# Kernel optimization log

Hardware: AMD Instinct MI355X
Metric: run time of the kernel (lower is better)

The kernel has to match this reference:

```python
import jax, jax.numpy as jnp
import numpy as np

B = 2; CIN = 64; COUT = 64; H = 192; W = 192
KH = 3; KW = 3; K = KH * KW; NC = 20
STRIDE = 1; PAD = 1; DIL = 1


def setup_inputs() -> dict:
    key = jax.random.key(0)
    ks = jax.random.split(key, 7)
    x = jax.random.normal(ks[0], (B, CIN, H, W), jnp.float32)
    input_LO = jax.random.uniform(ks[1], (B, NC, H, W), jnp.float32)
    output_LO = jax.random.uniform(ks[2], (B, NC, H, W), jnp.float32)  # HO=H, WO=W for k3 s1 p1
    weight = jax.random.normal(ks[3], (COUT, CIN, KH, KW), jnp.float32) * 0.05
    bias = jax.random.normal(ks[4], (COUT,), jnp.float32) * 0.05
    # conv_offset is zero-init in source; use small random weights so offsets are exercised
    off_w = jax.random.normal(ks[5], (2 * K, CIN, KH, KW), jnp.float32) * 0.01
    off_b = jnp.zeros((2 * K,), jnp.float32)
    return {"x": x, "input_LO": input_LO, "output_LO": output_LO,
            "weight": weight, "bias": bias, "off_w": off_w, "off_b": off_b}


def _gather(img_flat, idx):
    # img_flat: [B, C, H*W], idx: [B, N] -> [B, C, N]
    return jax.vmap(lambda im, ix: im[:, ix])(img_flat, idx)


def _bilinear(img, py, px, zero_pad):
    """Bilinear sample img [B,C,Hi,Wi] at pixel coords py/px [B,K,Ho,Wo].
    zero_pad=True -> zeros outside (deformable conv); False -> border clamp (grid_sample border)."""
    Bb, Cc, Hh, Ww = img.shape
    if not zero_pad:
        px = jnp.clip(px, 0.0, Ww - 1.0)
        py = jnp.clip(py, 0.0, Hh - 1.0)
    x0 = jnp.floor(px)
    y0 = jnp.floor(py)
    img_f = img.reshape(Bb, Cc, Hh * Ww)
    out = jnp.zeros((Bb, Cc) + px.shape[1:], img.dtype)
    for dy in (0.0, 1.0):
        for dx in (0.0, 1.0):
            yc = y0 + dy
            xc = x0 + dx
            w = (1.0 - jnp.abs(py - yc)) * (1.0 - jnp.abs(px - xc))
            if zero_pad:
                valid = (yc >= 0) & (yc <= Hh - 1) & (xc >= 0) & (xc <= Ww - 1)
                w = w * valid.astype(w.dtype)
            yi = jnp.clip(yc, 0, Hh - 1).astype(jnp.int32)
            xi = jnp.clip(xc, 0, Ww - 1).astype(jnp.int32)
            idx = (yi * Ww + xi).reshape(Bb, -1)
            g = _gather(img_f, idx).reshape((Bb, Cc) + px.shape[1:])
            out = out + g * w[:, None]
    return out


def reference(x, input_LO, output_LO, weight, bias, off_w, off_b):
    # 1) offset conv (torch chunk+cat is identity, so offset == conv_offset(x))
    offset = jax.lax.conv_general_dilated(
        x, off_w, (STRIDE, STRIDE), ((PAD, PAD), (PAD, PAD)),
        dimension_numbers=("NCHW", "OIHW", "NCHW")) + off_b[None, :, None, None]
    Bb, _, Ho, Wo = offset.shape
    off = offset.reshape(Bb, K, 2, Ho, Wo)
    off_y = off[:, :, 0]   # channel 2k   -> y offset
    off_x = off[:, :, 1]   # channel 2k+1 -> x offset
    hk = (jnp.arange(K) // KW).astype(x.dtype)[None, :, None, None]
    wk = (jnp.arange(K) % KW).astype(x.dtype)[None, :, None, None]

    # 2) mask: grid_sample label map at deformed locations (align_corners=True, border pad)
    hor = jnp.linspace(-1.0, 1.0, Wo)[None, None, None, :]
    ver = jnp.linspace(-1.0, 1.0, Ho)[None, None, :, None]
    gx = hor * STRIDE - PAD + (wk + off_x) / ((W - 1.0) / 2.0)
    gy = ver * STRIDE - PAD + (hk + off_y) / ((H - 1.0) / 2.0)
    px = (gx + 1.0) * (W - 1.0) / 2.0
    py = (gy + 1.0) * (H - 1.0) / 2.0
    samp_LO = _bilinear(input_LO, py, px, zero_pad=False)        # [B,NC,K,Ho,Wo]
    mask = jnp.einsum("bnkhw,bnhw->bkhw", samp_LO, output_LO)    # [B,K,Ho,Wo]

    # 3) modulated deformable conv (DCNv2 math, zero padding outside)
    base_y = (jnp.arange(Ho) * STRIDE - PAD).astype(x.dtype)[None, None, :, None]
    base_x = (jnp.arange(Wo) * STRIDE - PAD).astype(x.dtype)[None, None, None, :]
    py2 = base_y + hk * DIL + off_y
    px2 = base_x + wk * DIL + off_x
    samp = _bilinear(x, py2, px2, zero_pad=True)                 # [B,C,K,Ho,Wo]
    samp = samp * mask[:, None]
    out = jnp.einsum("bckhw,ock->bohw", samp, weight.reshape(COUT, CIN, K))
    return out + bias[None, :, None, None]
```

## Files before the change

kernel.cpp:

```cpp
#include <hip/hip_runtime.h>

#define Bn   2
#define CIN  64
#define COUT 64
#define Hd   192
#define Wd   192
#define HWd  (Hd*Wd)
#define Kk   9
#define NCh  20
#define NCP  24
#define NTILE 1152

typedef __attribute__((ext_vector_type(8))) short short8;
typedef __attribute__((ext_vector_type(4))) float f32x4;

static __device__ __forceinline__ ushort f2bf(float f) {
    unsigned u = __float_as_uint(f);
    u += 0x7fffu + ((u >> 16) & 1u);
    return (ushort)(u >> 16);
}
static __device__ __forceinline__ float bf2f(ushort v) {
    return __uint_as_float(((unsigned)v) << 16);
}

__global__ __launch_bounds__(256) void kT(const float* __restrict__ x,
        const float* __restrict__ inLO, const float* __restrict__ outLO,
        const float* __restrict__ w, const float* __restrict__ off_w,
        ushort* __restrict__ xtb, ushort* __restrict__ inLOb,
        ushort* __restrict__ outLOb, ushort* __restrict__ wtb,
        ushort* __restrict__ owtb) {
    __shared__ float lds[20 * 257];
    int bid = blockIdx.x, tid = threadIdx.x;
    if (bid < 1152) {
        int b = bid / 576, p0 = (bid % 576) * 64;
        const float* src = x + b * CIN * HWd + p0;
        #pragma unroll
        for (int r = 0; r < 16; ++r) {
            int e = r * 256 + tid;
            int c = e >> 6, p = e & 63;
            lds[c * 65 + p] = src[c * HWd + p];
        }
        __syncthreads();
        ushort* dst = xtb + ((size_t)(b * HWd + p0)) * 64;
        #pragma unroll
        for (int r = 0; r < 16; ++r) {
            int e = r * 256 + tid;
            int p = e >> 6, c = e & 63;
            dst[e] = f2bf(lds[c * 65 + p]);
        }
    } else if (bid < 1728) {
        int q = bid - 1152;
        int t = q / 288; q %= 288;
        int b = q / 144, p0 = (q % 144) * 256;
        const float* src = (t == 0 ? inLO : outLO) + b * NCh * HWd + p0;
        ushort* dst = (t == 0 ? inLOb : outLOb) + ((size_t)(b * HWd + p0)) * NCP;
        #pragma unroll
        for (int r = 0; r < 20; ++r) {
            int e = r * 256 + tid;
            int n = e >> 8, p = e & 255;
            lds[n * 257 + p] = src[n * HWd + p];
        }
        __syncthreads();
        #pragma unroll
        for (int r = 0; r < 24; ++r) {
            int e = r * 256 + tid;
            int p = e / NCP, n = e - p * NCP;
            dst[e] = (n < NCh) ? f2bf(lds[n * 257 + p]) : (ushort)0;
        }
    } else if (bid < 1872) {
        int f = (bid - 1728) * 256 + tid;
        int e = f & 7, lane = (f >> 3) & 63;
        int kt = (f >> 9) & 1, nt = (f >> 10) & 3, tap = f >> 12;
        int o = nt * 16 + (lane & 15);
        int c = kt * 32 + (lane >> 4) * 8 + e;
        wtb[f] = f2bf(w[(o * CIN + c) * Kk + tap]);
    } else {
        int f = (bid - 1872) * 256 + tid;
        if (f < 18432) {
            int e = f & 7, lane = (f >> 3) & 63;
            int kt = (f >> 9) & 1, nt = (f >> 10) & 1, tap = f >> 11;
            int oc = nt * 16 + (lane & 15);
            int c = kt * 32 + (lane >> 4) * 8 + e;
            owtb[f] = (oc < 18) ? f2bf(off_w[(oc * CIN + c) * Kk + tap]) : (ushort)0;
        }
    }
}

__global__ __launch_bounds__(256) void k1_gemm(const ushort* __restrict__ xtb,
        const ushort* __restrict__ owtb, const float* __restrict__ off_b,
        float* __restrict__ off) {
    int tid = threadIdx.x, bid = blockIdx.x;
    int jt = bid % 3, i = (bid / 3) % Hd, b = bid / (3 * Hd);
    int j0 = jt * 64;
    int lane = tid & 63, wv = tid >> 6;
    int m = lane & 15;
    int ch8 = lane >> 4;
    int j = j0 + wv * 16 + m;
    const ushort* xb = xtb + (size_t)b * HWd * 64;

    float bv0 = off_b[m];
    float bv1 = (m < 2) ? off_b[16 + m] : 0.f;
    f32x4 acc0 = (f32x4){bv0, bv0, bv0, bv0};
    f32x4 acc1 = (f32x4){bv1, bv1, bv1, bv1};
    short8 zero8 = {0, 0, 0, 0, 0, 0, 0, 0};

    #pragma unroll
    for (int t = 0; t < 9; ++t) {
        int yy = i + t / 3 - 1;
        int xx = j + t % 3 - 1;
        bool ok = (yy >= 0) && (yy < Hd) && (xx >= 0) && (xx < Wd);
        int yc = min(max(yy, 0), Hd - 1), xc = min(max(xx, 0), Wd - 1);
        const ushort* rowp = xb + (size_t)(yc * Wd + xc) * 64 + ch8 * 8;
        short8 a0 = *(const short8*)rowp;
        short8 a1 = *(const short8*)(rowp + 32);
        a0 = ok ? a0 : zero8;
        a1 = ok ? a1 : zero8;
        const ushort* wb = owtb + ((size_t)t << 11);
        short8 b00 = *(const short8*)(wb + (lane << 3));
        short8 b01 = *(const short8*)(wb + 512 + (lane << 3));
        short8 b10 = *(const short8*)(wb + 1024 + (lane << 3));
        short8 b11 = *(const short8*)(wb + 1536 + (lane << 3));
        acc0 = __builtin_amdgcn_mfma_f32_16x16x32_bf16(a0, b00, acc0, 0, 0, 0);
        acc0 = __builtin_amdgcn_mfma_f32_16x16x32_bf16(a1, b01, acc0, 0, 0, 0);
        acc1 = __builtin_amdgcn_mfma_f32_16x16x32_bf16(a0, b10, acc1, 0, 0, 0);
        acc1 = __builtin_amdgcn_mfma_f32_16x16x32_bf16(a1, b11, acc1, 0, 0, 0);
    }

    int prow = j0 + wv * 16 + (lane >> 4) * 4;
    int oc = lane & 15;
    float* ob = off + (size_t)b * 18 * HWd + i * Wd;
    #pragma unroll
    for (int r = 0; r < 4; ++r)
        ob[oc * HWd + prow + r] = acc0[r];
    if (oc < 2) {
        #pragma unroll
        for (int r = 0; r < 4; ++r)
            ob[(16 + oc) * HWd + prow + r] = acc1[r];
    }
}

__global__ __launch_bounds__(256) void k2_mask(const ushort* __restrict__ inLOb,
        const ushort* __restrict__ outLOb, const float* __restrict__ off,
        float* __restrict__ mask) {
    int t = blockIdx.x * 256 + threadIdx.x;
    int p = t % HWd;
    int k = (t / HWd) % Kk;
    int b = t / (Kk * HWd);
    int j = p % Wd, i = p / Wd;
    float offy = off[(b * 18 + 2 * k) * HWd + p];
    float offx = off[(b * 18 + 2 * k + 1) * HWd + p];
    float py = (float)(i + (k / 3)) + offy - 95.5f;
    float px = (float)(j + (k % 3)) + offx - 95.5f;
    py = fminf(fmaxf(py, 0.f), 191.f);
    px = fminf(fmaxf(px, 0.f), 191.f);
    float y0f = floorf(py), x0f = floorf(px);
    float ly = py - y0f, lx = px - x0f;
    int y0 = (int)y0f, x0 = (int)x0f;
    int y1 = min(y0 + 1, Hd - 1), x1 = min(x0 + 1, Wd - 1);
    float w00 = (1.f - ly) * (1.f - lx);
    float w01 = (1.f - ly) * lx;
    float w10 = ly * (1.f - lx);
    float w11 = ly * lx;
    const short8* L00 = (const short8*)(inLOb + (size_t)(b * HWd + y0 * Wd + x0) * NCP);
    const short8* L01 = (const short8*)(inLOb + (size_t)(b * HWd + y0 * Wd + x1) * NCP);
    const short8* L10 = (const short8*)(inLOb + (size_t)(b * HWd + y1 * Wd + x0) * NCP);
    const short8* L11 = (const short8*)(inLOb + (size_t)(b * HWd + y1 * Wd + x1) * NCP);
    const short8* O  = (const short8*)(outLOb + (size_t)(b * HWd + p) * NCP);
    float acc = 0.f;
    #pragma unroll
    for (int n3 = 0; n3 < 3; ++n3) {
        short8 a = L00[n3], bb = L01[n3], c = L10[n3], d = L11[n3], o = O[n3];
        #pragma unroll
        for (int e = 0; e < 8; ++e) {
            float s = w00 * bf2f((ushort)a[e]) + w01 * bf2f((ushort)bb[e])
                    + w10 * bf2f((ushort)c[e]) + w11 * bf2f((ushort)d[e]);
            acc += s * bf2f((ushort)o[e]);
        }
    }
    mask[(b * Kk + k) * HWd + p] = acc;
}

__global__ __launch_bounds__(256) void k3_part(const ushort* __restrict__ xtb,
        const float* __restrict__ off, const float* __restrict__ mask,
        const ushort* __restrict__ wtb, float* __restrict__ part) {
    __shared__ __align__(16) ushort A_lds[4 * 2 * 64 * 8];
    int tid = threadIdx.x;
    int bid = blockIdx.x;
    int h = bid >= NTILE;
    int tb = bid - (h ? NTILE : 0);
    int t0 = h ? 5 : 0, t1 = h ? 9 : 5;
    int jt = tb % 3, i = (tb / 3) % Hd, b = tb / (3 * Hd);
    int j0 = jt * 64;

    int lane = tid & 63;
    int wv_id = tid >> 6;
    int wm = wv_id >> 1;
    int wn = wv_id & 1;

    int pxo = lane & 7;
    int chunk = lane >> 3;
    int kt_s = chunk >> 2;
    int ksub = chunk & 3;
    const ushort* xb = xtb + (size_t)b * HWd * 64;

    f32x4 acc[2][2];
    #pragma unroll
    for (int mi = 0; mi < 2; ++mi)
        #pragma unroll
        for (int ni = 0; ni < 2; ++ni)
            acc[mi][ni] = (f32x4){0.f, 0.f, 0.f, 0.f};

    for (int t = t0; t < t1; ++t) {
        short8 bf[2][2];
        #pragma unroll
        for (int kt = 0; kt < 2; ++kt)
            #pragma unroll
            for (int ni = 0; ni < 2; ++ni) {
                int nt = wn * 2 + ni;
                bf[kt][ni] = *(const short8*)(wtb +
                    ((((t * 4 + nt) * 2 + kt) * 64 + lane) << 3));
            }

        #pragma unroll
        for (int r = 0; r < 2; ++r) {
            int px_loc = (wv_id << 4) + (r << 3) + pxo;
            int pix = i * Wd + j0 + px_loc;
            float offy = off[(b * 18 + 2 * t) * HWd + pix];
            float offx = off[(b * 18 + 2 * t + 1) * HWd + pix];
            float m = mask[(b * Kk + t) * HWd + pix];
            float py = (float)(i - 1 + (t / 3)) + offy;
            float px = (float)(j0 + px_loc - 1 + (t % 3)) + offx;
            float y0f = floorf(py), x0f = floorf(px);
            float ly = py - y0f, lx = px - x0f;
            int y0 = (int)y0f, x0 = (int)x0f;
            int y1 = y0 + 1, x1 = x0 + 1;
            bool vy0 = (y0 >= 0 && y0 < Hd), vy1 = (y1 >= 0 && y1 < Hd);
            bool vx0 = (x0 >= 0 && x0 < Wd), vx1 = (x1 >= 0 && x1 < Wd);
            float w00 = (vy0 && vx0) ? (1.f - ly) * (1.f - lx) * m : 0.f;
            float w01 = (vy0 && vx1) ? (1.f - ly) * lx * m : 0.f;
            float w10 = (vy1 && vx0) ? ly * (1.f - lx) * m : 0.f;
            float w11 = (vy1 && vx1) ? ly * lx * m : 0.f;
            int y0c = min(max(y0, 0), Hd - 1), y1c = min(max(y1, 0), Hd - 1);
            int x0c = min(max(x0, 0), Wd - 1), x1c = min(max(x1, 0), Wd - 1);
            const short8* g0p = (const short8*)(xb + (size_t)(y0c * Wd + x0c) * 64 + chunk * 8);
            const short8* g1p = (const short8*)(xb + (size_t)(y0c * Wd + x1c) * 64 + chunk * 8);
            const short8* g2p = (const short8*)(xb + (size_t)(y1c * Wd + x0c) * 64 + chunk * 8);
            const short8* g3p = (const short8*)(xb + (size_t)(y1c * Wd + x1c) * 64 + chunk * 8);
            short8 g0 = *g0p, g1 = *g1p, g2 = *g2p, g3 = *g3p;
            short8 pk;
            #pragma unroll
            for (int e = 0; e < 8; ++e) {
                float s = w00 * bf2f((ushort)g0[e]) + w01 * bf2f((ushort)g1[e])
                        + w10 * bf2f((ushort)g2[e]) + w11 * bf2f((ushort)g3[e]);
                pk[e] = (short)f2bf(s);
            }
            *(short8*)&A_lds[(((wv_id * 2 + kt_s) * 64 + ksub * 16 +
                               ((r << 3) + pxo)) << 3)] = pk;
        }
        __syncthreads();

        #pragma unroll
        for (int kt = 0; kt < 2; ++kt) {
            #pragma unroll
            for (int mi = 0; mi < 2; ++mi) {
                int mt2 = wm * 2 + mi;
                short8 af = *(const short8*)&A_lds[(((mt2 * 2 + kt) * 64 + lane) << 3)];
                acc[mi][0] = __builtin_amdgcn_mfma_f32_16x16x32_bf16(
                                 af, bf[kt][0], acc[mi][0], 0, 0, 0);
                acc[mi][1] = __builtin_amdgcn_mfma_f32_16x16x32_bf16(
                                 af, bf[kt][1], acc[mi][1], 0, 0, 0);
            }
        }
        __syncthreads();
    }

    float* pb = part + ((size_t)(h * NTILE + tb) << 12);
    int colo = lane & 15;
    int rb = (lane >> 4) * 4;
    #pragma unroll
    for (int ni = 0; ni < 2; ++ni) {
        int o = wn * 32 + ni * 16 + colo;
        #pragma unroll
        for (int mi = 0; mi < 2; ++mi) {
            int p0 = wm * 32 + mi * 16 + rb;
            float4 r;
            r.x = acc[mi][ni][0];
            r.y = acc[mi][ni][1];
            r.z = acc[mi][ni][2];
            r.w = acc[mi][ni][3];
            *(float4*)(pb + o * 64 + p0) = r;
        }
    }
}

__global__ __launch_bounds__(256) void k4_reduce(const float* __restrict__ part,
        const float* __restrict__ bias, float* __restrict__ out) {
    int e4 = blockIdx.x * 256 + threadIdx.x;
    int tile = e4 >> 10;
    int wi = e4 & 1023;
    int o = wi >> 4;
    int p0 = (wi & 15) << 2;
    const float4* pp = (const float4*)part;
    float4 a = pp[e4];
    float4 c = pp[e4 + NTILE * 1024];
    float bv = bias[o];
    int jt = tile % 3, i = (tile / 3) % Hd, b = tile / (3 * Hd);
    float4 r;
    r.x = a.x + c.x + bv;
    r.y = a.y + c.y + bv;
    r.z = a.z + c.z + bv;
    r.w = a.w + c.w + bv;
    *(float4*)(out + ((size_t)(b * COUT + o) * HWd) + i * Wd + jt * 64 + p0) = r;
}

extern "C" void kernel_launch(void* const* d_in, const int* in_sizes, int n_in,
                              void* d_out, int out_size, void* d_ws, size_t ws_size,
                              hipStream_t stream) {
    const float* x      = (const float*)d_in[0];
    const float* inLO   = (const float*)d_in[1];
    const float* outLO  = (const float*)d_in[2];
    const float* weight = (const float*)d_in[3];
    const float* bias   = (const float*)d_in[4];
    const float* off_w  = (const float*)d_in[5];
    const float* off_b  = (const float*)d_in[6];
    float* out = (float*)d_out;

    float*  off    = (float*)d_ws;
    float*  mask   = off   + Bn * 18 * HWd;
    ushort* wtb    = (ushort*)(mask + Bn * Kk * HWd);
    ushort* owtb   = wtb + 36864;
    ushort* xtb    = owtb + 18432;
    ushort* inLOb  = xtb + (size_t)Bn * HWd * CIN;
    ushort* outLOb = inLOb + (size_t)Bn * HWd * NCP;
    float*  part   = (float*)(outLOb + (size_t)Bn * HWd * NCP);

    kT<<<1944, 256, 0, stream>>>(x, inLO, outLO, weight, off_w,
                                 xtb, inLOb, outLOb, wtb, owtb);
    k1_gemm<<<NTILE, 256, 0, stream>>>(xtb, owtb, off_b, off);
    k2_mask<<<2592, 256, 0, stream>>>(inLOb, outLOb, off, mask);
    k3_part<<<2 * NTILE, 256, 0, stream>>>(xtb, off, mask, wtb, part);
    k4_reduce<<<4608, 256, 0, stream>>>(part, bias, out);
}
```

Measured before the change: 174.6 us.

## Precompute deform-conv sampling records in mask kernel and store partials as bf16

```diff
diff --git a/kernel.cpp b/kernel.cpp
--- a/kernel.cpp
+++ b/kernel.cpp
@@ -1,4 +1,5 @@
 #include <hip/hip_runtime.h>
+#include <hip/hip_fp16.h>
 
 #define Bn   2
 #define CIN  64
@@ -21,6 +22,12 @@
 }
 static __device__ __forceinline__ float bf2f(ushort v) {
     return __uint_as_float(((unsigned)v) << 16);
+}
+static __device__ __forceinline__ ushort f2h(float f) {
+    return __half_as_ushort(__float2half_rn(f));
+}
+static __device__ __forceinline__ float h2f(ushort u) {
+    return __half2float(__ushort_as_half(u));
 }
 
 __global__ __launch_bounds__(256) void kT(const float* __restrict__ x,
@@ -141,7 +148,7 @@
 
 __global__ __launch_bounds__(256) void k2_mask(const ushort* __restrict__ inLOb,
         const ushort* __restrict__ outLOb, const float* __restrict__ off,
-        float* __restrict__ mask) {
+        uint4* __restrict__ rec) {
     int t = blockIdx.x * 256 + threadIdx.x;
     int p = t % HWd;
     int k = (t / HWd) % Kk;
@@ -149,6 +156,7 @@
     int j = p % Wd, i = p / Wd;
     float offy = off[(b * 18 + 2 * k) * HWd + p];
     float offx = off[(b * 18 + 2 * k + 1) * HWd + p];
+
     float py = (float)(i + (k / 3)) + offy - 95.5f;
     float px = (float)(j + (k % 3)) + offx - 95.5f;
     py = fminf(fmaxf(py, 0.f), 191.f);
@@ -177,12 +185,32 @@
             acc += s * bf2f((ushort)o[e]);
         }
     }
-    mask[(b * Kk + k) * HWd + p] = acc;
+
+    float py2 = (float)(i - 1 + (k / 3)) + offy;
+    float px2 = (float)(j - 1 + (k % 3)) + offx;
+    float y0f2 = floorf(py2), x0f2 = floorf(px2);
+    float ly2 = py2 - y0f2, lx2 = px2 - x0f2;
+    int yA = (int)y0f2, xA = (int)x0f2;
+    int yB = yA + 1, xB = xA + 1;
+    bool vy0 = (yA >= 0 && yA < Hd), vy1 = (yB >= 0 && yB < Hd);
+    bool vx0 = (xA >= 0 && xA < Wd), vx1 = (xB >= 0 && xB < Wd);
+    float W00 = (vy0 && vx0) ? (1.f - ly2) * (1.f - lx2) * acc : 0.f;
+    float W01 = (vy0 && vx1) ? (1.f - ly2) * lx2 * acc : 0.f;
+    float W10 = (vy1 && vx0) ? ly2 * (1.f - lx2) * acc : 0.f;
+    float W11 = (vy1 && vx1) ? ly2 * lx2 * acc : 0.f;
+    int y0c = min(max(yA, 0), Hd - 1), y1c = min(max(yB, 0), Hd - 1);
+    int x0c = min(max(xA, 0), Wd - 1), x1c = min(max(xB, 0), Wd - 1);
+    uint4 r;
+    r.x = (unsigned)y0c | ((unsigned)y1c << 16);
+    r.y = (unsigned)x0c | ((unsigned)x1c << 16);
+    r.z = (unsigned)f2h(W00) | ((unsigned)f2h(W01) << 16);
+    r.w = (unsigned)f2h(W10) | ((unsigned)f2h(W11) << 16);
+    rec[(size_t)(b * Kk + k) * HWd + p] = r;
 }
 
 __global__ __launch_bounds__(256) void k3_part(const ushort* __restrict__ xtb,
-        const float* __restrict__ off, const float* __restrict__ mask,
-        const ushort* __restrict__ wtb, float* __restrict__ part) {
+        const uint4* __restrict__ rec, const ushort* __restrict__ wtb,
+        ushort* __restrict__ part) {
     __shared__ __align__(16) ushort A_lds[4 * 2 * 64 * 8];
     int tid = threadIdx.x;
     int bid = blockIdx.x;
@@ -221,31 +249,21 @@
                     ((((t * 4 + nt) * 2 + kt) * 64 + lane) << 3));
             }
 
+        const uint4* recb = rec + (size_t)(b * Kk + t) * HWd + i * Wd + j0;
         #pragma unroll
         for (int r = 0; r < 2; ++r) {
             int px_loc = (wv_id << 4) + (r << 3) + pxo;
-            int pix = i * Wd + j0 + px_loc;
-            float offy = off[(b * 18 + 2 * t) * HWd + pix];
-            float offx = off[(b * 18 + 2 * t + 1) * HWd + pix];
-            float m = mask[(b * Kk + t) * HWd + pix];
-            float py = (float)(i - 1 + (t / 3)) + offy;
-            float px = (float)(j0 + px_loc - 1 + (t % 3)) + offx;
-            float y0f = floorf(py), x0f = floorf(px);
-            float ly = py - y0f, lx = px - x0f;
-            int y0 = (int)y0f, x0 = (int)x0f;
-            int y1 = y0 + 1, x1 = x0 + 1;
-            bool vy0 = (y0 >= 0 && y0 < Hd), vy1 = (y1 >= 0 && y1 < Hd);
-            bool vx0 = (x0 >= 0 && x0 < Wd), vx1 = (x1 >= 0 && x1 < Wd);
-            float w00 = (vy0 && vx0) ? (1.f - ly) * (1.f - lx) * m : 0.f;
-            float w01 = (vy0 && vx1) ? (1.f - ly) * lx * m : 0.f;
-            float w10 = (vy1 && vx0) ? ly * (1.f - lx) * m : 0.f;
-            float w11 = (vy1 && vx1) ? ly * lx * m : 0.f;
-            int y0c = min(max(y0, 0), Hd - 1), y1c = min(max(y1, 0), Hd - 1);
-            int x0c = min(max(x0, 0), Wd - 1), x1c = min(max(x1, 0), Wd - 1);
-            const short8* g0p = (const short8*)(xb + (size_t)(y0c * Wd + x0c) * 64 + chunk * 8);
-            const short8* g1p = (const short8*)(xb + (size_t)(y0c * Wd + x1c) * 64 + chunk * 8);
-            const short8* g2p = (const short8*)(xb + (size_t)(y1c * Wd + x0c) * 64 + chunk * 8);
-            const short8* g3p = (const short8*)(xb + (size_t)(y1c * Wd + x1c) * 64 + chunk * 8);
+            uint4 rc = recb[px_loc];
+            int y0 = rc.x & 0xffff, y1 = rc.x >> 16;
+            int x0 = rc.y & 0xffff, x1 = rc.y >> 16;
+            float w00 = h2f((ushort)(rc.z & 0xffff));
+            float w01 = h2f((ushort)(rc.z >> 16));
+            float w10 = h2f((ushort)(rc.w & 0xffff));
+            float w11 = h2f((ushort)(rc.w >> 16));
+            const short8* g0p = (const short8*)(xb + (size_t)(y0 * Wd + x0) * 64 + chunk * 8);
+            const short8* g1p = (const short8*)(xb + (size_t)(y0 * Wd + x1) * 64 + chunk * 8);
+            const short8* g2p = (const short8*)(xb + (size_t)(y1 * Wd + x0) * 64 + chunk * 8);
+            const short8* g3p = (const short8*)(xb + (size_t)(y1 * Wd + x1) * 64 + chunk * 8);
             short8 g0 = *g0p, g1 = *g1p, g2 = *g2p, g3 = *g3p;
             short8 pk;
             #pragma unroll
@@ -274,7 +292,7 @@
         __syncthreads();
     }
 
-    float* pb = part + ((size_t)(h * NTILE + tb) << 12);
+    ushort* pb = part + ((size_t)(h * NTILE + tb) << 12);
     int colo = lane & 15;
     int rb = (lane >> 4) * 4;
     #pragma unroll
@@ -283,34 +301,40 @@
         #pragma unroll
         for (int mi = 0; mi < 2; ++mi) {
             int p0 = wm * 32 + mi * 16 + rb;
-            float4 r;
-            r.x = acc[mi][ni][0];
-            r.y = acc[mi][ni][1];
-            r.z = acc[mi][ni][2];
-            r.w = acc[mi][ni][3];
-            *(float4*)(pb + o * 64 + p0) = r;
-        }
-    }
-}
-
-__global__ __launch_bounds__(256) void k4_reduce(const float* __restrict__ part,
+            ushort4 s;
+            s.x = f2bf(acc[mi][ni][0]);
+            s.y = f2bf(acc[mi][ni][1]);
+            s.z = f2bf(acc[mi][ni][2]);
+            s.w = f2bf(acc[mi][ni][3]);
+            *(ushort4*)(pb + o * 64 + p0) = s;
+        }
+    }
+}
+
+__global__ __launch_bounds__(256) void k4_reduce(const ushort* __restrict__ part,
         const float* __restrict__ bias, float* __restrict__ out) {
-    int e4 = blockIdx.x * 256 + threadIdx.x;
-    int tile = e4 >> 10;
-    int wi = e4 & 1023;
-    int o = wi >> 4;
-    int p0 = (wi & 15) << 2;
-    const float4* pp = (const float4*)part;
-    float4 a = pp[e4];
-    float4 c = pp[e4 + NTILE * 1024];
+    int g = blockIdx.x * 256 + threadIdx.x;
+    int tile = g >> 9;
+    int wi = g & 511;
+    int o = wi >> 3;
+    int p0 = (wi & 7) << 3;
+    const short8* pp = (const short8*)part;
+    short8 a = pp[g];
+    short8 c = pp[g + NTILE * 512];
     float bv = bias[o];
     int jt = tile % 3, i = (tile / 3) % Hd, b = tile / (3 * Hd);
-    float4 r;
-    r.x = a.x + c.x + bv;
-    r.y = a.y + c.y + bv;
-    r.z = a.z + c.z + bv;
-    r.w = a.w + c.w + bv;
-    *(float4*)(out + ((size_t)(b * COUT + o) * HWd) + i * Wd + jt * 64 + p0) = r;
+    float* op = out + ((size_t)(b * COUT + o) * HWd) + i * Wd + jt * 64 + p0;
+    float4 r0, r1;
+    r0.x = bf2f((ushort)a[0]) + bf2f((ushort)c[0]) + bv;
+    r0.y = bf2f((ushort)a[1]) + bf2f((ushort)c[1]) + bv;
+    r0.z = bf2f((ushort)a[2]) + bf2f((ushort)c[2]) + bv;
+    r0.w = bf2f((ushort)a[3]) + bf2f((ushort)c[3]) + bv;
+    r1.x = bf2f((ushort)a[4]) + bf2f((ushort)c[4]) + bv;
+    r1.y = bf2f((ushort)a[5]) + bf2f((ushort)c[5]) + bv;
+    r1.z = bf2f((ushort)a[6]) + bf2f((ushort)c[6]) + bv;
+    r1.w = bf2f((ushort)a[7]) + bf2f((ushort)c[7]) + bv;
+    *(float4*)op = r0;
+    *(float4*)(op + 4) = r1;
 }
 
 extern "C" void kernel_launch(void* const* d_in, const int* in_sizes, int n_in,
@@ -325,19 +349,19 @@
     const float* off_b  = (const float*)d_in[6];
     float* out = (float*)d_out;
 
-    float*  off    = (float*)d_ws;
-    float*  mask   = off   + Bn * 18 * HWd;
-    ushort* wtb    = (ushort*)(mask + Bn * Kk * HWd);
+    uint4*  rec    = (uint4*)d_ws;
+    ushort* part   = (ushort*)(rec + (size_t)Bn * Kk * HWd);
+    float*  off    = (float*)(part + (size_t)2 * NTILE * 4096);
+    ushort* wtb    = (ushort*)(off + (size_t)Bn * 18 * HWd);
     ushort* owtb   = wtb + 36864;
     ushort* xtb    = owtb + 18432;
     ushort* inLOb  = xtb + (size_t)Bn * HWd * CIN;
     ushort* outLOb = inLOb + (size_t)Bn * HWd * NCP;
-    float*  part   = (float*)(outLOb + (size_t)Bn * HWd * NCP);
 
     kT<<<1944, 256, 0, stream>>>(x, inLO, outLO, weight, off_w,
                                  xtb, inLOb, outLOb, wtb, owtb);
     k1_gemm<<<NTILE, 256, 0, stream>>>(xtb, owtb, off_b, off);
-    k2_mask<<<2592, 256, 0, stream>>>(inLOb, outLOb, off, mask);
-    k3_part<<<2 * NTILE, 256, 0, stream>>>(xtb, off, mask, wtb, part);
-    k4_reduce<<<4608, 256, 0, stream>>>(part, bias, out);
-}
+    k2_mask<<<2592, 256, 0, stream>>>(inLOb, outLOb, off, rec);
+    k3_part<<<2 * NTILE, 256, 0, stream>>>(xtb, rec, wtb, part);
+    k4_reduce<<<2304, 256, 0, stream>>>(part, bias, out);
+}
```

Measured after the change: 173.7 us. No clear change (-0.5%).
